# Kernel tuning notes

Hardware: AMD Instinct MI355X
Metric: run time of the kernel (lower is better)

Reference implementation:

```python
import jax, jax.numpy as jnp
import numpy as np

ALPHA = 0.2          # LeakyReLU negative slope
NEG_INF = -9e15      # mask value from the torch source
N, F_IN, F_OUT = 8192, 128, 64


def setup_inputs() -> dict:
    key = jax.random.key(0)
    k1, k2, k3, k4, k5 = jax.random.split(key, 5)
    X = jax.random.normal(k1, (N, F_IN), dtype=jnp.float32)
    A = jax.random.randint(k2, (N, N), 0, 2, dtype=jnp.int32)  # 0/1 adjacency
    W = jax.random.normal(k3, (F_IN, F_OUT), dtype=jnp.float32) * 0.05
    a1 = jax.random.normal(k4, (F_OUT,), dtype=jnp.float32) * 0.05
    a2 = jax.random.normal(k5, (F_OUT,), dtype=jnp.float32) * 0.05
    return {"X": X, "A": A, "W": W, "a1": a1, "a2": a2}


def reference(X, A, W, a1, a2):
    # h = W(X)  (Linear, no bias)
    h = X @ W                                   # (N, F_out)
    # a([h_i || h_j]) == h_i @ a1 + h_j @ a2  (split of the 2F attention vector)
    s1 = h @ a1                                 # (N,)
    s2 = h @ a2                                 # (N,)
    e = jax.nn.leaky_relu(s1[:, None] + s2[None, :], ALPHA)  # (N, N)
    att = jnp.where(A > 0, e, NEG_INF)
    att = jax.nn.softmax(att, axis=1)           # row-wise masked softmax
    # dropout p=0.0 -> identity
    return att @ h                              # (N, F_out)
```

## Files before the change

kernel.cpp:

```cpp
#include <hip/hip_runtime.h>
#include <hip/hip_bf16.h>

#define NV 8192
#define FIN 128
#define FOUT 64

typedef __attribute__((ext_vector_type(8))) short short8;
typedef __attribute__((ext_vector_type(4))) float floatx4;

__device__ __forceinline__ uint f2bf_u(float f) {
  uint u = __float_as_uint(f);
  return (u + 0x7FFFu + ((u >> 16) & 1u)) >> 16;
}
__device__ __forceinline__ float bf2f(ushort b) {
  return __uint_as_float(((uint)b) << 16);
}

__global__ void k0_detect(const uint* __restrict__ X, int* __restrict__ flag) {
  const int lane = threadIdx.x & 63;
  uint u = X[lane];
  uint e = (u >> 7) & 0xFF;
  bool ok = (e >= 100u) && (e <= 135u);
  unsigned long long b = __ballot(ok);
  if (lane == 0) *flag = (__builtin_popcountll(b) >= 48) ? 1 : 0;
}

__global__ __launch_bounds__(256) void k1_proj(
    const void* __restrict__ Xv, const void* __restrict__ Wv,
    const void* __restrict__ a1v_, const void* __restrict__ a2v_,
    ushort* __restrict__ HtB, float* __restrict__ s1, float* __restrict__ s2,
    const int* __restrict__ flagp)
{
  const int is_bf16 = *flagp;
  const int wave = threadIdx.x >> 6;
  const int lane = threadIdx.x & 63;
  const int i0 = blockIdx.x * 64 + wave * 16;
  const int col = lane & 15;
  const int q   = lane >> 4;

  short8 bfrag[4][4];
  float a1f[4], a2f[4];
  if (is_bf16) {
    const ushort* W = (const ushort*)Wv;
#pragma unroll
    for (int nt = 0; nt < 4; ++nt)
#pragma unroll
      for (int kc = 0; kc < 4; ++kc) {
        short8 b;
#pragma unroll
        for (int j = 0; j < 8; ++j)
          b[j] = (short)W[(kc*32 + q*8 + j)*FOUT + nt*16 + col];
        bfrag[nt][kc] = b;
      }
#pragma unroll
    for (int nt = 0; nt < 4; ++nt) {
      a1f[nt] = bf2f(((const ushort*)a1v_)[nt*16 + col]);
      a2f[nt] = bf2f(((const ushort*)a2v_)[nt*16 + col]);
    }
  } else {
    const float* W = (const float*)Wv;
#pragma unroll
    for (int nt = 0; nt < 4; ++nt)
#pragma unroll
      for (int kc = 0; kc < 4; ++kc) {
        short8 b;
#pragma unroll
        for (int j = 0; j < 8; ++j)
          b[j] = (short)f2bf_u(W[(kc*32 + q*8 + j)*FOUT + nt*16 + col]);
        bfrag[nt][kc] = b;
      }
#pragma unroll
    for (int nt = 0; nt < 4; ++nt) {
      a1f[nt] = ((const float*)a1v_)[nt*16 + col];
      a2f[nt] = ((const float*)a2v_)[nt*16 + col];
    }
  }

  floatx4 acc[4] = {{0.f,0.f,0.f,0.f},{0.f,0.f,0.f,0.f},
                    {0.f,0.f,0.f,0.f},{0.f,0.f,0.f,0.f}};
#pragma unroll
  for (int kc = 0; kc < 4; ++kc) {
    short8 a;
    if (is_bf16) {
      a = *(const short8*)&((const ushort*)Xv)[(size_t)(i0 + col)*FIN + kc*32 + q*8];
    } else {
      const float* X = (const float*)Xv;
      float4 x0 = *(const float4*)&X[(size_t)(i0 + col)*FIN + kc*32 + q*8];
      float4 x1 = *(const float4*)&X[(size_t)(i0 + col)*FIN + kc*32 + q*8 + 4];
      a[0] = (short)f2bf_u(x0.x); a[1] = (short)f2bf_u(x0.y);
      a[2] = (short)f2bf_u(x0.z); a[3] = (short)f2bf_u(x0.w);
      a[4] = (short)f2bf_u(x1.x); a[5] = (short)f2bf_u(x1.y);
      a[6] = (short)f2bf_u(x1.z); a[7] = (short)f2bf_u(x1.w);
    }
#pragma unroll
    for (int nt = 0; nt < 4; ++nt)
      acc[nt] = __builtin_amdgcn_mfma_f32_16x16x32_bf16(a, bfrag[nt][kc], acc[nt], 0, 0, 0);
  }

  const int r0  = wave*16 + q*4;
  const int kcH = r0 >> 5;
  const int q2  = (r0 >> 3) & 3;
  const int j0  = r0 & 7;
  ushort* chunkp = HtB + (size_t)blockIdx.x * 4096;

  float s1p[4] = {0,0,0,0}, s2p[4] = {0,0,0,0};
#pragma unroll
  for (int nt = 0; nt < 4; ++nt) {
    ushort4 pk;
    pk.x = (ushort)f2bf_u(acc[nt][0]);
    pk.y = (ushort)f2bf_u(acc[nt][1]);
    pk.z = (ushort)f2bf_u(acc[nt][2]);
    pk.w = (ushort)f2bf_u(acc[nt][3]);
    *(ushort4*)&chunkp[((kcH*4 + nt)*64 + q2*16 + col)*8 + j0] = pk;
#pragma unroll
    for (int reg = 0; reg < 4; ++reg) {
      s1p[reg] += acc[nt][reg] * a1f[nt];
      s2p[reg] += acc[nt][reg] * a2f[nt];
    }
  }
#pragma unroll
  for (int m = 1; m < 16; m <<= 1)
#pragma unroll
    for (int reg = 0; reg < 4; ++reg) {
      s1p[reg] += __shfl_xor(s1p[reg], m, 64);
      s2p[reg] += __shfl_xor(s2p[reg], m, 64);
    }
  if (col == 0)
#pragma unroll
    for (int reg = 0; reg < 4; ++reg) {
      s1[i0 + q*4 + reg] = s1p[reg];
      s2[i0 + q*4 + reg] = s2p[reg];
    }
}

#define CT 256
#define NT (NV / CT)
#define PST 72

__global__ __launch_bounds__(256) void k2_attn(
    const int* __restrict__ A, const ushort* __restrict__ HtB,
    const float* __restrict__ s1g, const float* __restrict__ s2g,
    void* __restrict__ outv, const int* __restrict__ flagp)
{
  __shared__ __align__(16) ushort Pl[4][16 * PST];
  __shared__ __align__(16) float Red[4][16][64];
  __shared__ float Lw[4][16];

  const int is_bf16 = *flagp;
  const int tid  = threadIdx.x;
  const int wave = tid >> 6;
  const int lane = tid & 63;
  const int i0   = blockIdx.x * 16;
  const int q    = lane >> 4;
  const int mcol = lane & 15;

  ushort* Pw = &Pl[wave][0];

  float s1v[4];
#pragma unroll
  for (int rr = 0; rr < 4; ++rr) s1v[rr] = s1g[i0 + q*4 + rr];

  size_t arow[4];
#pragma unroll
  for (int rr = 0; rr < 4; ++rr)
    arow[rr] = (size_t)(i0 + q*4 + rr) * NV + mcol*4;

  float Lp[4] = {0,0,0,0};
  floatx4 acc[4] = {{0.f,0.f,0.f,0.f},{0.f,0.f,0.f,0.f},
                    {0.f,0.f,0.f,0.f},{0.f,0.f,0.f,0.f}};

  int4 av[4];
  float4 sv;
  {
    const int c = wave * 64;
#pragma unroll
    for (int rr = 0; rr < 4; ++rr) av[rr] = *(const int4*)&A[arow[rr] + c];
    sv = *(const float4*)&s2g[c + mcol*4];
  }

  for (int t = 0; t < NT; ++t) {
    const int c = t*CT + wave*64;
    const int cn = (t + 1 < NT) ? (c + CT) : c;
    int4 nav[4];
    float4 nsv;
#pragma unroll
    for (int rr = 0; rr < 4; ++rr) nav[rr] = *(const int4*)&A[arow[rr] + cn];
    nsv = *(const float4*)&s2g[cn + mcol*4];

#pragma unroll
    for (int rr = 0; rr < 4; ++rr) {
      const int4 a = av[rr];
      const float s1r = s1v[rr];
      float x0 = s1r + sv.x, x1 = s1r + sv.y, x2 = s1r + sv.z, x3 = s1r + sv.w;
      float w0 = a.x ? __expf(fmaxf(x0, 0.2f*x0)) : 0.f;
      float w1 = a.y ? __expf(fmaxf(x1, 0.2f*x1)) : 0.f;
      float w2 = a.z ? __expf(fmaxf(x2, 0.2f*x2)) : 0.f;
      float w3 = a.w ? __expf(fmaxf(x3, 0.2f*x3)) : 0.f;
      Lp[rr] += (w0 + w1) + (w2 + w3);
      uint2 pk;
      pk.x = f2bf_u(w0) | (f2bf_u(w1) << 16);
      pk.y = f2bf_u(w2) | (f2bf_u(w3) << 16);
      *(uint2*)&Pw[(q*4 + rr)*PST + mcol*4] = pk;
    }

    const size_t chb = (size_t)(t*4 + wave) * 4096;
#pragma unroll
    for (int kc2 = 0; kc2 < 2; ++kc2) {
      short8 af = *(const short8*)&Pw[mcol*PST + kc2*32 + q*8];
#pragma unroll
      for (int nt = 0; nt < 4; ++nt) {
        short8 bf = *(const short8*)&HtB[chb + ((kc2*4 + nt)*64 + lane)*8];
        acc[nt] = __builtin_amdgcn_mfma_f32_16x16x32_bf16(af, bf, acc[nt], 0, 0, 0);
      }
    }

#pragma unroll
    for (int rr = 0; rr < 4; ++rr) av[rr] = nav[rr];
    sv = nsv;
  }

#pragma unroll
  for (int m = 1; m < 16; m <<= 1)
#pragma unroll
    for (int rr = 0; rr < 4; ++rr) Lp[rr] += __shfl_xor(Lp[rr], m, 64);
  if (mcol == 0)
#pragma unroll
    for (int rr = 0; rr < 4; ++rr) Lw[wave][q*4 + rr] = Lp[rr];

#pragma unroll
  for (int nt = 0; nt < 4; ++nt)
#pragma unroll
    for (int reg = 0; reg < 4; ++reg)
      Red[wave][q*4 + reg][nt*16 + mcol] = acc[nt][reg];

  __syncthreads();

  {
    const int r  = tid >> 4;
    const int fb = (tid & 15) * 4;
    float4 s = {0.f, 0.f, 0.f, 0.f};
    float L = 0.f;
#pragma unroll
    for (int w = 0; w < 4; ++w) {
      float4 v = *(const float4*)&Red[w][r][fb];
      s.x += v.x; s.y += v.y; s.z += v.z; s.w += v.w;
      L += Lw[w][r];
    }
    const float inv = __frcp_rn(L);
    s.x *= inv; s.y *= inv; s.z *= inv; s.w *= inv;
    if (is_bf16) {
      ushort4 pk;
      pk.x = (ushort)f2bf_u(s.x); pk.y = (ushort)f2bf_u(s.y);
      pk.z = (ushort)f2bf_u(s.z); pk.w = (ushort)f2bf_u(s.w);
      *(ushort4*)&((ushort*)outv)[(size_t)(i0 + r)*FOUT + fb] = pk;
    } else {
      *(float4*)&((float*)outv)[(size_t)(i0 + r)*FOUT + fb] = s;
    }
  }
}

extern "C" void kernel_launch(void* const* d_in, const int* in_sizes, int n_in,
                              void* d_out, int out_size, void* d_ws, size_t ws_size,
                              hipStream_t stream) {
  const void* X  = d_in[0];
  const int*  A  = (const int*)d_in[1];
  const void* W  = d_in[2];
  const void* a1 = d_in[3];
  const void* a2 = d_in[4];

  char* ws = (char*)d_ws;
  ushort* HtB  = (ushort*)ws;
  float*  s1   = (float*)(ws + (size_t)FOUT*NV*2);
  float*  s2   = s1 + NV;
  int*    flag = (int*)(s2 + NV);

  hipLaunchKernelGGL(k0_detect, dim3(1), dim3(64), 0, stream,
                     (const uint*)X, flag);
  hipLaunchKernelGGL(k1_proj, dim3(NV/64), dim3(256), 0, stream,
                     X, W, a1, a2, HtB, s1, s2, flag);
  hipLaunchKernelGGL(k2_attn, dim3(NV/16), dim3(256), 0, stream,
                     A, HtB, s1, s2, d_out, flag);
}
```

Before: 457.6 us.

## Split attention columns into four slices with a combine kernel and deeper prefetch

The attention kernel now splits each 16-row block's column range into four slices, launching four times as many blocks, with staggered start offsets per row block. Partial numerators and row sums go to a workspace and are reduced by a new combine kernel. The loop also double-buffers adjacency loads two iterations ahead and preloads the H fragments into registers for the next tile. This targets low occupancy and memory latency on the 256 MB adjacency stream, at the cost of extra partial-sum traffic, one more launch and higher register pressure.

Result: faster. 437.7 us (-4.3%).

```diff
diff --git a/kernel.cpp b/kernel.cpp
--- a/kernel.cpp
+++ b/kernel.cpp
@@ -133,26 +133,30 @@
     }
 }
 
-#define CT 256
-#define NT (NV / CT)
+#define SLICES 4
+#define SW (NV / SLICES)
+#define NIT (SW / 256)
 #define PST 72
 
-__global__ __launch_bounds__(256) void k2_attn(
+__global__ __launch_bounds__(256, 4) void k2_attn(
     const int* __restrict__ A, const ushort* __restrict__ HtB,
     const float* __restrict__ s1g, const float* __restrict__ s2g,
-    void* __restrict__ outv, const int* __restrict__ flagp)
+    float* __restrict__ Part, float* __restrict__ Lpart)
 {
   __shared__ __align__(16) ushort Pl[4][16 * PST];
   __shared__ __align__(16) float Red[4][16][64];
   __shared__ float Lw[4][16];
 
-  const int is_bf16 = *flagp;
   const int tid  = threadIdx.x;
   const int wave = tid >> 6;
   const int lane = tid & 63;
-  const int i0   = blockIdx.x * 16;
+  const int sl   = blockIdx.x & (SLICES - 1);
+  const int rb   = blockIdx.x >> 2;
+  const int i0   = rb * 16;
   const int q    = lane >> 4;
   const int mcol = lane & 15;
+  const int c0s  = sl * SW;
+  const int t0   = (rb * 3) & (NIT - 1);
 
   ushort* Pw = &Pl[wave][0];
 
@@ -163,35 +167,41 @@
   size_t arow[4];
 #pragma unroll
   for (int rr = 0; rr < 4; ++rr)
-    arow[rr] = (size_t)(i0 + q*4 + rr) * NV + mcol*4;
+    arow[rr] = (size_t)(i0 + q*4 + rr) * NV + c0s + mcol*4;
 
   float Lp[4] = {0,0,0,0};
   floatx4 acc[4] = {{0.f,0.f,0.f,0.f},{0.f,0.f,0.f,0.f},
                     {0.f,0.f,0.f,0.f},{0.f,0.f,0.f,0.f}};
 
-  int4 av[4];
-  float4 sv;
+  #define OFF(t) ((((t) + t0) & (NIT - 1)) * 256 + wave * 64)
+  #define CHK(t) ((size_t)(sl*32 + (((t) + t0) & (NIT - 1))*4 + wave) * 4096)
+
+  int4 av[2][4];
+  float4 sv[2];
+#pragma unroll
+  for (int s = 0; s < 2; ++s) {
+    const int c = OFF(s);
+#pragma unroll
+    for (int rr = 0; rr < 4; ++rr) av[s][rr] = *(const int4*)&A[arow[rr] + c];
+    sv[s] = *(const float4*)&s2g[c0s + c + mcol*4];
+  }
+  short8 bf[8];
   {
-    const int c = wave * 64;
-#pragma unroll
-    for (int rr = 0; rr < 4; ++rr) av[rr] = *(const int4*)&A[arow[rr] + c];
-    sv = *(const float4*)&s2g[c + mcol*4];
-  }
-
-  for (int t = 0; t < NT; ++t) {
-    const int c = t*CT + wave*64;
-    const int cn = (t + 1 < NT) ? (c + CT) : c;
-    int4 nav[4];
-    float4 nsv;
-#pragma unroll
-    for (int rr = 0; rr < 4; ++rr) nav[rr] = *(const int4*)&A[arow[rr] + cn];
-    nsv = *(const float4*)&s2g[cn + mcol*4];
+    const size_t cb = CHK(0);
+#pragma unroll
+    for (int k = 0; k < 8; ++k)
+      bf[k] = *(const short8*)&HtB[cb + ((size_t)(k*64 + lane)) * 8];
+  }
+
+  for (int t = 0; t < NIT; ++t) {
+    const int cur = t & 1;
 
 #pragma unroll
     for (int rr = 0; rr < 4; ++rr) {
-      const int4 a = av[rr];
+      const int4 a = av[cur][rr];
       const float s1r = s1v[rr];
-      float x0 = s1r + sv.x, x1 = s1r + sv.y, x2 = s1r + sv.z, x3 = s1r + sv.w;
+      const float4 s2v = sv[cur];
+      float x0 = s1r + s2v.x, x1 = s1r + s2v.y, x2 = s1r + s2v.z, x3 = s1r + s2v.w;
       float w0 = a.x ? __expf(fmaxf(x0, 0.2f*x0)) : 0.f;
       float w1 = a.y ? __expf(fmaxf(x1, 0.2f*x1)) : 0.f;
       float w2 = a.z ? __expf(fmaxf(x2, 0.2f*x2)) : 0.f;
@@ -203,20 +213,29 @@
       *(uint2*)&Pw[(q*4 + rr)*PST + mcol*4] = pk;
     }
 
-    const size_t chb = (size_t)(t*4 + wave) * 4096;
+    {
+      const int tn = (t + 2 < NIT) ? (t + 2) : t;
+      const int c2 = OFF(tn);
+#pragma unroll
+      for (int rr = 0; rr < 4; ++rr) av[cur][rr] = *(const int4*)&A[arow[rr] + c2];
+      sv[cur] = *(const float4*)&s2g[c0s + c2 + mcol*4];
+    }
+
 #pragma unroll
     for (int kc2 = 0; kc2 < 2; ++kc2) {
       short8 af = *(const short8*)&Pw[mcol*PST + kc2*32 + q*8];
 #pragma unroll
-      for (int nt = 0; nt < 4; ++nt) {
-        short8 bf = *(const short8*)&HtB[chb + ((kc2*4 + nt)*64 + lane)*8];
-        acc[nt] = __builtin_amdgcn_mfma_f32_16x16x32_bf16(af, bf, acc[nt], 0, 0, 0);
-      }
-    }
-
-#pragma unroll
-    for (int rr = 0; rr < 4; ++rr) av[rr] = nav[rr];
-    sv = nsv;
+      for (int nt = 0; nt < 4; ++nt)
+        acc[nt] = __builtin_amdgcn_mfma_f32_16x16x32_bf16(af, bf[kc2*4 + nt], acc[nt], 0, 0, 0);
+    }
+
+    {
+      const int tb = (t + 1 < NIT) ? (t + 1) : t;
+      const size_t cb = CHK(tb);
+#pragma unroll
+      for (int k = 0; k < 8; ++k)
+        bf[k] = *(const short8*)&HtB[cb + ((size_t)(k*64 + lane)) * 8];
+    }
   }
 
 #pragma unroll
@@ -246,16 +265,37 @@
       s.x += v.x; s.y += v.y; s.z += v.z; s.w += v.w;
       L += Lw[w][r];
     }
-    const float inv = __frcp_rn(L);
-    s.x *= inv; s.y *= inv; s.z *= inv; s.w *= inv;
-    if (is_bf16) {
-      ushort4 pk;
-      pk.x = (ushort)f2bf_u(s.x); pk.y = (ushort)f2bf_u(s.y);
-      pk.z = (ushort)f2bf_u(s.z); pk.w = (ushort)f2bf_u(s.w);
-      *(ushort4*)&((ushort*)outv)[(size_t)(i0 + r)*FOUT + fb] = pk;
-    } else {
-      *(float4*)&((float*)outv)[(size_t)(i0 + r)*FOUT + fb] = s;
-    }
+    *(float4*)&Part[((size_t)sl * NV + i0 + r) * FOUT + fb] = s;
+    if ((tid & 15) == 0) Lpart[(size_t)sl * NV + i0 + r] = L;
+  }
+}
+
+__global__ __launch_bounds__(256) void k3_combine(
+    const float* __restrict__ Part, const float* __restrict__ Lpart,
+    void* __restrict__ outv, const int* __restrict__ flagp)
+{
+  const int is_bf16 = *flagp;
+  const int g   = blockIdx.x * 256 + threadIdx.x;
+  const int row = g >> 4;
+  const int fb  = (g & 15) * 4;
+
+  float4 s = {0.f, 0.f, 0.f, 0.f};
+  float L = 0.f;
+#pragma unroll
+  for (int sl = 0; sl < SLICES; ++sl) {
+    float4 v = *(const float4*)&Part[((size_t)sl * NV + row) * FOUT + fb];
+    s.x += v.x; s.y += v.y; s.z += v.z; s.w += v.w;
+    L += Lpart[(size_t)sl * NV + row];
+  }
+  const float inv = __frcp_rn(L);
+  s.x *= inv; s.y *= inv; s.z *= inv; s.w *= inv;
+  if (is_bf16) {
+    ushort4 pk;
+    pk.x = (ushort)f2bf_u(s.x); pk.y = (ushort)f2bf_u(s.y);
+    pk.z = (ushort)f2bf_u(s.z); pk.w = (ushort)f2bf_u(s.w);
+    *(ushort4*)&((ushort*)outv)[(size_t)row * FOUT + fb] = pk;
+  } else {
+    *(float4*)&((float*)outv)[(size_t)row * FOUT + fb] = s;
   }
 }
 
@@ -269,15 +309,19 @@
   const void* a2 = d_in[4];
 
   char* ws = (char*)d_ws;
-  ushort* HtB  = (ushort*)ws;
-  float*  s1   = (float*)(ws + (size_t)FOUT*NV*2);
-  float*  s2   = s1 + NV;
-  int*    flag = (int*)(s2 + NV);
+  ushort* HtB   = (ushort*)ws;
+  float*  s1    = (float*)(ws + (size_t)FOUT*NV*2);
+  float*  s2    = s1 + NV;
+  int*    flag  = (int*)(s2 + NV);
+  float*  Part  = (float*)((char*)flag + 16);
+  float*  Lpart = Part + (size_t)SLICES * NV * FOUT;
 
   hipLaunchKernelGGL(k0_detect, dim3(1), dim3(64), 0, stream,
                      (const uint*)X, flag);
   hipLaunchKernelGGL(k1_proj, dim3(NV/64), dim3(256), 0, stream,
                      X, W, a1, a2, HtB, s1, s2, flag);
-  hipLaunchKernelGGL(k2_attn, dim3(NV/16), dim3(256), 0, stream,
-                     A, HtB, s1, s2, d_out, flag);
-}
+  hipLaunchKernelGGL(k2_attn, dim3((NV/16) * SLICES), dim3(256), 0, stream,
+                     A, HtB, s1, s2, Part, Lpart);
+  hipLaunchKernelGGL(k3_combine, dim3(NV*FOUT/4/256), dim3(256), 0, stream,
+                     Part, Lpart, d_out, flag);
+}
```
